# Kernel optimization log

Measured on AMD Instinct MI355X. Metric: run time of the kernel, lower is better.

Reference implementation:

```python
import jax, jax.numpy as jnp
import numpy as np

B, N, C, M, OUT = 4, 256, 32, 4, 64


def _uniform(k, shape, fan_in):
    s = 1.0 / np.sqrt(fan_in)
    return jax.random.uniform(k, shape, jnp.float32, -s, s)


def setup_inputs() -> dict:
    key = jax.random.key(0)
    ks = jax.random.split(key, 11)
    return {
        "x": jax.random.normal(ks[0], (B, N, N, C), jnp.float32),
        # Neighborhood / SnConv2to1 linears (in=C, out=M neighborhood channels)
        "w1_nb": _uniform(ks[1], (3 * C, M), 3 * C),
        "b1_nb": _uniform(ks[2], (M,), 3 * C),
        "w0_nb": _uniform(ks[3], (2 * C, M), 2 * C),
        "b0_nb": _uniform(ks[4], (M,), 2 * C),
        # SnConv2 linears (in channels = M*C after neighborhood product)
        "w2d": _uniform(ks[5], (2 * M * C, OUT), 2 * M * C),
        "b2d": _uniform(ks[6], (OUT,), 2 * M * C),
        "w1d": _uniform(ks[7], (3 * M * C, OUT), 3 * M * C),
        "b1d": _uniform(ks[8], (OUT,), 3 * M * C),
        "w0d": _uniform(ks[9], (2 * M * C, OUT), 2 * M * C),
        "b0d": _uniform(ks[10], (OUT,), 2 * M * C),
    }


def _contractions(x):
    # x: [B, n, n, c]; mask=None, reduction='mean' path of _get_contractions
    n = x.shape[1]
    rowsum = x.sum(axis=1) / n                      # [B, n, c]
    colsum = x.sum(axis=2) / n                      # [B, n, c]
    diag = jnp.diagonal(x, axis1=1, axis2=2)        # [B, c, n]
    rowcolsum = x.sum(axis=(1, 2)) / (n * n)        # [B, c]
    diag_sum = diag.sum(axis=-1) / n                # [B, c]  (/= sqrt(n^2))
    diag = jnp.moveaxis(diag, -1, 1)                # move_from_end -> [B, n, c]
    return rowsum, colsum, diag, rowcolsum, diag_sum


def reference(x, w1_nb, b1_nb, w0_nb, b0_nb, w2d, b2d, w1d, b1d, w0d, b0d):
    # ---- Neighborhood: SnConv2to1 -> sigmoid ----
    rs, cs, dg, rcs, ds = _contractions(x)
    obj1 = jnp.concatenate([rs, cs, dg], axis=-1)             # [B, n, 3C]
    obj0 = jnp.concatenate([rcs, ds], axis=-1)                # [B, 2C]
    node = obj1 @ w1_nb + b1_nb + (obj0 @ w0_nb + b0_nb)[:, None, :]
    neighbs = jax.nn.sigmoid(node)                            # [B, n, M]
    # ---- _neighbor_elementwise_product ----
    expanded = neighbs[:, None, :, :] * neighbs[:, :, None, :]  # [B, n, n, M]
    # channel_product: outer product over channel dims, collapsed to M*C
    xl = (expanded[..., :, None] * x[..., None, :]).reshape(B, N, N, M * C)
    # ---- SnConv2 on the localized tensor ----
    rs2, cs2, dg2, rcs2, ds2 = _contractions(xl)
    obj2d = jnp.concatenate([xl, jnp.swapaxes(xl, 1, 2)], axis=-1)  # [B,n,n,2MC]
    obj1d = jnp.concatenate([rs2, cs2, dg2], axis=-1)               # [B,n,3MC]
    obj0d = jnp.concatenate([rcs2, ds2], axis=-1)                   # [B,2MC]
    out = (obj2d @ w2d + b2d
           + (obj1d @ w1d + b1d)[:, None, :, :]
           + (obj0d @ w0d + b0d)[:, None, None, :])                 # [B,n,n,OUT]
    return out
```

## Files before the change

### kernel.cpp

```cpp
#include <hip/hip_runtime.h>
#include <math.h>

#define Bv 4
#define Nv 256
#define Cv 32
#define Mv 4
#define OUTv 64
#define MCv (Mv*Cv)

typedef _Float16 h8 __attribute__((ext_vector_type(8)));
typedef _Float16 h4 __attribute__((ext_vector_type(4)));
typedef float f4 __attribute__((ext_vector_type(4)));

__device__ __align__(16) float g_rs  [Bv * Nv * Cv];
__device__ __align__(16) float g_cs  [Bv * Nv * Cv];
__device__ __align__(16) float g_dgx [Bv * Nv * Cv];
__device__ __align__(16) float g_nb  [Bv * Nv * Mv];
__device__ __align__(16) float g_S1  [Bv * Nv * MCv];
__device__ __align__(16) float g_S2  [Bv * Nv * MCv];
__device__ __align__(16) float g_rcs2R[8 * Bv * MCv];
__device__ __align__(16) float g_ds2R [8 * Bv * MCv];
__device__ __align__(16) float g_addv[Bv * Nv * OUTv];
__device__ __align__(16) _Float16 g_wfrag[8 * 4 * 64 * 8];

__global__ __launch_bounds__(256) void k_contract1(const float* __restrict__ x,
                                                   const float* __restrict__ w2d) {
    int bx = blockIdx.x, b = blockIdx.y;
    int t = threadIdx.x;
    if (bx >= 2 * Nv) {
        if (b != 0) return;
        int r = bx - 2 * Nv;
        if (r == 8) {
            float4 z = {0.f,0.f,0.f,0.f};
            #pragma unroll
            for (int k = 0; k < 4; k++) {
                ((float4*)g_rcs2R)[k * 256 + t] = z;
                ((float4*)g_ds2R )[k * 256 + t] = z;
            }
            return;
        }
        int fi = r * 256 + t;
        int s = fi >> 8, q = (fi >> 6) & 3, lane = fi & 63;
        int k0 = s * 32 + ((lane >> 4) << 3);
        int o = q * 16 + (lane & 15);
        #pragma unroll
        for (int jj = 0; jj < 8; jj++)
            g_wfrag[fi * 8 + jj] = (_Float16)w2d[(size_t)(k0 + jj) * OUTv + o];
        return;
    }
    int c4 = t & 7, sub = t >> 3;
    const float4* xb4 = (const float4*)(x + (size_t)b * Nv * Nv * Cv);
    __shared__ float red[32][36];
    float4 acc = {0.f,0.f,0.f,0.f};
    if (bx < Nv) {
        int n = bx;
        for (int i = sub; i < Nv; i += 32) {
            float4 v = xb4[((size_t)i * Nv + n) * 8 + c4];
            acc.x += v.x; acc.y += v.y; acc.z += v.z; acc.w += v.w;
        }
        red[sub][c4*4+0] = acc.x; red[sub][c4*4+1] = acc.y;
        red[sub][c4*4+2] = acc.z; red[sub][c4*4+3] = acc.w;
        __syncthreads();
        if (t < 32) {
            float s = 0.f;
            #pragma unroll
            for (int k = 0; k < 32; k++) s += red[k][t];
            g_rs[(b * Nv + n) * Cv + t] = s * (1.0f / Nv);
        }
        if (t < 8) ((float4*)g_dgx)[(b * Nv + n) * 8 + t] = xb4[((size_t)n * Nv + n) * 8 + t];
    } else {
        int n = bx - Nv;
        for (int j = sub; j < Nv; j += 32) {
            float4 v = xb4[((size_t)n * Nv + j) * 8 + c4];
            acc.x += v.x; acc.y += v.y; acc.z += v.z; acc.w += v.w;
        }
        red[sub][c4*4+0] = acc.x; red[sub][c4*4+1] = acc.y;
        red[sub][c4*4+2] = acc.z; red[sub][c4*4+3] = acc.w;
        __syncthreads();
        if (t < 32) {
            float s = 0.f;
            #pragma unroll
            for (int k = 0; k < 32; k++) s += red[k][t];
            g_cs[(b * Nv + n) * Cv + t] = s * (1.0f / Nv);
        }
    }
}

__global__ void k_neighb(const float* __restrict__ w1, const float* __restrict__ b1,
                         const float* __restrict__ w0, const float* __restrict__ b0) {
    int b = blockIdx.x, t = threadIdx.x;
    int c = t & 31, sub = t >> 5;
    float ar = 0.f, ad = 0.f;
    for (int n = sub; n < Nv; n += 8) {
        ar += g_rs[(b * Nv + n) * Cv + c];
        ad += g_dgx[(b * Nv + n) * Cv + c];
    }
    __shared__ float red[8][64];
    __shared__ float obj0[64];
    __shared__ float t0nb[4];
    red[sub][c] = ar;
    red[sub][32 + c] = ad;
    __syncthreads();
    if (t < 64) {
        float s = 0.f;
        #pragma unroll
        for (int k = 0; k < 8; k++) s += red[k][t];
        obj0[t] = s * (1.0f / Nv);
    }
    __syncthreads();
    if (t < 4) {
        float v = b0[t];
        for (int k = 0; k < 2 * Cv; k++) v += obj0[k] * w0[k * Mv + t];
        t0nb[t] = v;
    }
    __syncthreads();
    int n = t;
    float node[4];
    #pragma unroll
    for (int m = 0; m < 4; m++) node[m] = t0nb[m] + b1[m];
    for (int cc = 0; cc < Cv; cc++) {
        float r = g_rs[(b * Nv + n) * Cv + cc];
        float s = g_cs[(b * Nv + n) * Cv + cc];
        float d = g_dgx[(b * Nv + n) * Cv + cc];
        #pragma unroll
        for (int m = 0; m < 4; m++)
            node[m] += r * w1[cc * Mv + m] + s * w1[(Cv + cc) * Mv + m] + d * w1[(2 * Cv + cc) * Mv + m];
    }
    #pragma unroll
    for (int m = 0; m < 4; m++)
        g_nb[(b * Nv + n) * Mv + m] = 1.0f / (1.0f + expf(-node[m]));
}

__global__ __launch_bounds__(256) void k_wsum(const float* __restrict__ x) {
    int bx = blockIdx.x, b = blockIdx.y;
    int t = threadIdx.x, c4 = t & 7, sub = t >> 3;
    __shared__ __align__(16) float4 nbl[Nv];
    if (t < Nv) nbl[t] = ((const float4*)(g_nb + (size_t)b * Nv * Mv))[t];
    __syncthreads();
    const float4* xb4 = (const float4*)(x + (size_t)b * Nv * Nv * Cv);
    float4 a[4];
    #pragma unroll
    for (int m = 0; m < 4; m++) a[m] = {0.f,0.f,0.f,0.f};
    __shared__ float red[32][132];
    if (bx < Nv) {
        int n = bx;
        for (int i = sub; i < Nv; i += 32) {
            float4 v = xb4[((size_t)i * Nv + n) * 8 + c4];
            float4 nv = nbl[i];
            a[0].x += nv.x*v.x; a[0].y += nv.x*v.y; a[0].z += nv.x*v.z; a[0].w += nv.x*v.w;
            a[1].x += nv.y*v.x; a[1].y += nv.y*v.y; a[1].z += nv.y*v.z; a[1].w += nv.y*v.w;
            a[2].x += nv.z*v.x; a[2].y += nv.z*v.y; a[2].z += nv.z*v.z; a[2].w += nv.z*v.w;
            a[3].x += nv.w*v.x; a[3].y += nv.w*v.y; a[3].z += nv.w*v.z; a[3].w += nv.w*v.w;
        }
        #pragma unroll
        for (int m = 0; m < 4; m++) {
            red[sub][m*32 + c4*4+0] = a[m].x; red[sub][m*32 + c4*4+1] = a[m].y;
            red[sub][m*32 + c4*4+2] = a[m].z; red[sub][m*32 + c4*4+3] = a[m].w;
        }
        __syncthreads();
        if (t < 128) {
            float s = 0.f;
            #pragma unroll
            for (int k = 0; k < 32; k++) s += red[k][t];
            g_S1[(size_t)(b * Nv + n) * MCv + t] = s;
            int m = t >> 5, c = t & 31;
            float nv = ((const float*)&nbl[n])[m];
            int rep = ((n & 7) * Bv + b) * MCv + t;
            atomicAdd(&g_rcs2R[rep], nv * s);
            atomicAdd(&g_ds2R [rep], nv * nv * g_dgx[(b * Nv + n) * Cv + c]);
        }
    } else {
        int n = bx - Nv;
        for (int j = sub; j < Nv; j += 32) {
            float4 v = xb4[((size_t)n * Nv + j) * 8 + c4];
            float4 nv = nbl[j];
            a[0].x += nv.x*v.x; a[0].y += nv.x*v.y; a[0].z += nv.x*v.z; a[0].w += nv.x*v.w;
            a[1].x += nv.y*v.x; a[1].y += nv.y*v.y; a[1].z += nv.y*v.z; a[1].w += nv.y*v.w;
            a[2].x += nv.z*v.x; a[2].y += nv.z*v.y; a[2].z += nv.z*v.z; a[2].w += nv.z*v.w;
            a[3].x += nv.w*v.x; a[3].y += nv.w*v.y; a[3].z += nv.w*v.z; a[3].w += nv.w*v.w;
        }
        #pragma unroll
        for (int m = 0; m < 4; m++) {
            red[sub][m*32 + c4*4+0] = a[m].x; red[sub][m*32 + c4*4+1] = a[m].y;
            red[sub][m*32 + c4*4+2] = a[m].z; red[sub][m*32 + c4*4+3] = a[m].w;
        }
        __syncthreads();
        if (t < 128) {
            float s = 0.f;
            #pragma unroll
            for (int k = 0; k < 32; k++) s += red[k][t];
            g_S2[(size_t)(b * Nv + n) * MCv + t] = s;
        }
    }
}

__global__ __launch_bounds__(256) void k_add(const float* __restrict__ w1d,
                                             const float* __restrict__ b1d,
                                             const float* __restrict__ b2d,
                                             const float* __restrict__ w0d,
                                             const float* __restrict__ b0d) {
    int b = blockIdx.y, n0 = blockIdx.x * 2;
    int t = threadIdx.x, o = t & 63, ks = t >> 6;
    __shared__ float rcl[MCv], dsl[MCv];
    __shared__ float red0[4][64];
    __shared__ float red2[4][2][64];
    if (t < 128) {
        float s = 0.f;
        #pragma unroll
        for (int r = 0; r < 8; r++) s += g_rcs2R[(r * Bv + b) * MCv + t];
        rcl[t] = s;
    } else {
        int tt = t - 128;
        float s = 0.f;
        #pragma unroll
        for (int r = 0; r < 8; r++) s += g_ds2R[(r * Bv + b) * MCv + tt];
        dsl[tt] = s;
    }
    __syncthreads();
    const float invN = 1.0f / Nv;
    const float invN2 = invN * invN;
    float nv0 = g_nb[(b * Nv + n0) * Mv + ks];
    float nv1 = g_nb[(b * Nv + n0 + 1) * Mv + ks];
    float f0 = nv0 * invN, d20 = nv0 * nv0;
    float f1 = nv1 * invN, d21 = nv1 * nv1;
    const float* S1a = g_S1 + (size_t)(b * Nv + n0) * MCv + ks * 32;
    const float* S1b = S1a + MCv;
    const float* S2a = g_S2 + (size_t)(b * Nv + n0) * MCv + ks * 32;
    const float* S2b = S2a + MCv;
    const float* dga = g_dgx + (size_t)(b * Nv + n0) * Cv;
    const float* dgb = dga + Cv;
    float acc0v = 0.f, accA = 0.f, accB = 0.f;
    #pragma unroll 8
    for (int cc = 0; cc < 32; cc++) {
        int mc = ks * 32 + cc;
        float w1a = w1d[(size_t)mc * OUTv + o];
        float w1b = w1d[(size_t)(MCv + mc) * OUTv + o];
        float w1c = w1d[(size_t)(2 * MCv + mc) * OUTv + o];
        float w0a = w0d[(size_t)mc * OUTv + o];
        float w0b = w0d[(size_t)(MCv + mc) * OUTv + o];
        acc0v += invN2 * rcl[mc] * w0a + invN * dsl[mc] * w0b;
        accA  += f0 * S1a[cc] * w1a + f0 * S2a[cc] * w1b + d20 * dga[cc] * w1c;
        accB  += f1 * S1b[cc] * w1a + f1 * S2b[cc] * w1b + d21 * dgb[cc] * w1c;
    }
    red0[ks][o] = acc0v;
    red2[ks][0][o] = accA;
    red2[ks][1][o] = accB;
    __syncthreads();
    if (t < 128) {
        int nn = t >> 6, oo = t & 63;
        float t0v = red0[0][oo] + red0[1][oo] + red0[2][oo] + red0[3][oo]
                  + b1d[oo] + b2d[oo] + b0d[oo];
        float v = red2[0][nn][oo] + red2[1][nn][oo] + red2[2][nn][oo] + red2[3][nn][oo] + t0v;
        g_addv[(size_t)(b * Nv + n0 + nn) * OUTv + oo] = v;
    }
}

#define XPAD 40
__global__ __launch_bounds__(256) void k_main(const float* __restrict__ x,
                                              float* __restrict__ out) {
    int jt = blockIdx.x, ip = blockIdx.y, b = blockIdx.z;
    int i0 = ip * 2, i1 = i0 + 1;
    int j0 = jt * 128;
    int t = threadIdx.x;
    int lane = t & 63, w = t >> 6;
    int rowA = lane & 15, quad = lane >> 4;

    __shared__ __align__(16) _Float16 Wl[8 * 4 * 64 * 8];
    __shared__ __align__(16) _Float16 Xt0[128 * XPAD];
    __shared__ __align__(16) _Float16 Xb0[128 * XPAD];
    __shared__ __align__(16) _Float16 Xt1[128 * XPAD];
    __shared__ __align__(16) _Float16 Xb1[128 * XPAD];

    {
        const float4* src = (const float4*)g_wfrag;
        float4* dst = (float4*)Wl;
        #pragma unroll
        for (int r = 0; r < 8; r++) dst[r * 256 + t] = src[r * 256 + t];
    }
    {
        const float4* x4 = (const float4*)x;
        #pragma unroll
        for (int r = 0; r < 4; r++) {
            int idx = r * 256 + t;
            int j = idx >> 3, c4 = idx & 7;
            float4 v0 = x4[((size_t)(b * Nv + i0) * Nv + j0 + j) * 8 + c4];
            float4 v1 = x4[((size_t)(b * Nv + i1) * Nv + j0 + j) * 8 + c4];
            float4 u0 = x4[((size_t)(b * Nv + j0 + j) * Nv + i0) * 8 + c4];
            float4 u1 = x4[((size_t)(b * Nv + j0 + j) * Nv + i1) * 8 + c4];
            h4 h0; h0[0] = (_Float16)v0.x; h0[1] = (_Float16)v0.y;
            h0[2] = (_Float16)v0.z; h0[3] = (_Float16)v0.w;
            *(h4*)&Xt0[j * XPAD + c4 * 4] = h0;
            h4 h1; h1[0] = (_Float16)v1.x; h1[1] = (_Float16)v1.y;
            h1[2] = (_Float16)v1.z; h1[3] = (_Float16)v1.w;
            *(h4*)&Xt1[j * XPAD + c4 * 4] = h1;
            h4 g0; g0[0] = (_Float16)u0.x; g0[1] = (_Float16)u0.y;
            g0[2] = (_Float16)u0.z; g0[3] = (_Float16)u0.w;
            *(h4*)&Xb0[j * XPAD + c4 * 4] = g0;
            h4 g1; g1[0] = (_Float16)u1.x; g1[1] = (_Float16)u1.y;
            g1[2] = (_Float16)u1.z; g1[3] = (_Float16)u1.w;
            *(h4*)&Xb1[j * XPAD + c4 * 4] = g1;
        }
    }
    int jl1 = w * 32 + rowA, jl2 = jl1 + 16;
    _Float16 e1h0[4], e2h0[4], e1h1[4], e2h1[4];
    {
        const float* ni0 = g_nb + (size_t)(b * Nv + i0) * Mv;
        const float* ni1 = g_nb + (size_t)(b * Nv + i1) * Mv;
        const float* n1 = g_nb + (size_t)(b * Nv + j0 + jl1) * Mv;
        const float* n2 = g_nb + (size_t)(b * Nv + j0 + jl2) * Mv;
        #pragma unroll
        for (int m = 0; m < 4; m++) {
            e1h0[m] = (_Float16)(ni0[m] * n1[m]);
            e2h0[m] = (_Float16)(ni0[m] * n2[m]);
            e1h1[m] = (_Float16)(ni1[m] * n1[m]);
            e2h1[m] = (_Float16)(ni1[m] * n2[m]);
        }
    }
    __syncthreads();

    f4 acc[2][2][4];
    #pragma unroll
    for (int ii = 0; ii < 2; ii++)
        #pragma unroll
        for (int js = 0; js < 2; js++)
            #pragma unroll
            for (int q = 0; q < 4; q++) acc[ii][js][q] = {0.f, 0.f, 0.f, 0.f};

    const h8* Wf = (const h8*)Wl;
    #pragma unroll
    for (int part = 0; part < 2; part++) {
        const _Float16* X0 = part ? Xb0 : Xt0;
        const _Float16* X1 = part ? Xb1 : Xt1;
        h8 xv1_0 = *(const h8*)&X0[jl1 * XPAD + quad * 8];
        h8 xv2_0 = *(const h8*)&X0[jl2 * XPAD + quad * 8];
        h8 xv1_1 = *(const h8*)&X1[jl1 * XPAD + quad * 8];
        h8 xv2_1 = *(const h8*)&X1[jl2 * XPAD + quad * 8];
        #pragma unroll
        for (int m = 0; m < 4; m++) {
            h8 a1_0 = xv1_0 * e1h0[m];
            h8 a2_0 = xv2_0 * e2h0[m];
            h8 a1_1 = xv1_1 * e1h1[m];
            h8 a2_1 = xv2_1 * e2h1[m];
            int s = part * 4 + m;
            #pragma unroll
            for (int q = 0; q < 4; q++) {
                h8 bf = Wf[(s * 4 + q) * 64 + lane];
                acc[0][0][q] = __builtin_amdgcn_mfma_f32_16x16x32_f16(a1_0, bf, acc[0][0][q], 0, 0, 0);
                acc[0][1][q] = __builtin_amdgcn_mfma_f32_16x16x32_f16(a2_0, bf, acc[0][1][q], 0, 0, 0);
                acc[1][0][q] = __builtin_amdgcn_mfma_f32_16x16x32_f16(a1_1, bf, acc[1][0][q], 0, 0, 0);
                acc[1][1][q] = __builtin_amdgcn_mfma_f32_16x16x32_f16(a2_1, bf, acc[1][1][q], 0, 0, 0);
            }
        }
    }
    #pragma unroll
    for (int js = 0; js < 2; js++) {
        int jbase = j0 + w * 32 + js * 16 + quad * 4;
        #pragma unroll
        for (int q = 0; q < 4; q++) {
            int o = q * 16 + rowA;
            #pragma unroll
            for (int r = 0; r < 4; r++) {
                int j = jbase + r;
                float av = g_addv[(size_t)(b * Nv + j) * OUTv + o];
                out[(((size_t)(b * Nv + i0)) * Nv + j) * OUTv + o] = acc[0][js][q][r] + av;
                out[(((size_t)(b * Nv + i1)) * Nv + j) * OUTv + o] = acc[1][js][q][r] + av;
            }
        }
    }
}

extern "C" void kernel_launch(void* const* d_in, const int* in_sizes, int n_in,
                              void* d_out, int out_size, void* d_ws, size_t ws_size,
                              hipStream_t stream) {
    const float* x     = (const float*)d_in[0];
    const float* w1_nb = (const float*)d_in[1];
    const float* b1_nb = (const float*)d_in[2];
    const float* w0_nb = (const float*)d_in[3];
    const float* b0_nb = (const float*)d_in[4];
    const float* w2d   = (const float*)d_in[5];
    const float* b2d   = (const float*)d_in[6];
    const float* w1d   = (const float*)d_in[7];
    const float* b1d   = (const float*)d_in[8];
    const float* w0d   = (const float*)d_in[9];
    const float* b0d   = (const float*)d_in[10];
    float* out = (float*)d_out;
    (void)d_ws; (void)ws_size;

    hipLaunchKernelGGL(k_contract1, dim3(2 * Nv + 9, Bv), dim3(256), 0, stream, x, w2d);
    hipLaunchKernelGGL(k_neighb, dim3(Bv), dim3(256), 0, stream,
                       w1_nb, b1_nb, w0_nb, b0_nb);
    hipLaunchKernelGGL(k_wsum, dim3(2 * Nv, Bv), dim3(256), 0, stream, x);
    hipLaunchKernelGGL(k_add, dim3(Nv / 2, Bv), dim3(256), 0, stream,
                       w1d, b1d, b2d, w0d, b0d);
    hipLaunchKernelGGL(k_main, dim3(2, Nv / 2, Bv), dim3(256), 0, stream, x, out);
}
```

Baseline: 169.4 us.

## Fuse neighborhood, weighted-sum and per-row add kernels into one kernel

Merges k_neighb, k_wsum and k_add into a single k_fused kernel with one block per (n, b). Each block recomputes the sigmoid neighborhood weights for its batch, then computes both the row and column weighted sums and the per-row linear term from shared memory. This removes two launches and the global S1/S2 round-trip. The rcs2/ds2 reduction and its w0d product move into k_main, because the atomic accumulation must finish before they can be used. The cost is redundant neighborhood computation in every block and extra per-block setup work in k_main.

```diff
diff --git a/kernel.cpp b/kernel.cpp
--- a/kernel.cpp
+++ b/kernel.cpp
@@ -16,8 +16,6 @@
 __device__ __align__(16) float g_cs  [Bv * Nv * Cv];
 __device__ __align__(16) float g_dgx [Bv * Nv * Cv];
 __device__ __align__(16) float g_nb  [Bv * Nv * Mv];
-__device__ __align__(16) float g_S1  [Bv * Nv * MCv];
-__device__ __align__(16) float g_S2  [Bv * Nv * MCv];
 __device__ __align__(16) float g_rcs2R[8 * Bv * MCv];
 __device__ __align__(16) float g_ds2R [8 * Bv * MCv];
 __device__ __align__(16) float g_addv[Bv * Nv * OUTv];
@@ -86,25 +84,37 @@
     }
 }
 
-__global__ void k_neighb(const float* __restrict__ w1, const float* __restrict__ b1,
-                         const float* __restrict__ w0, const float* __restrict__ b0) {
-    int b = blockIdx.x, t = threadIdx.x;
-    int c = t & 31, sub = t >> 5;
-    float ar = 0.f, ad = 0.f;
-    for (int n = sub; n < Nv; n += 8) {
-        ar += g_rs[(b * Nv + n) * Cv + c];
-        ad += g_dgx[(b * Nv + n) * Cv + c];
-    }
-    __shared__ float red[8][64];
+__global__ __launch_bounds__(256) void k_fused(const float* __restrict__ x,
+    const float* __restrict__ w1, const float* __restrict__ b1,
+    const float* __restrict__ w0, const float* __restrict__ b0,
+    const float* __restrict__ w1d, const float* __restrict__ b1d,
+    const float* __restrict__ b2d, const float* __restrict__ b0d) {
+    int n = blockIdx.x, b = blockIdx.y;
+    int t = threadIdx.x;
+
+    __shared__ float red8[8][64];
     __shared__ float obj0[64];
     __shared__ float t0nb[4];
-    red[sub][c] = ar;
-    red[sub][32 + c] = ad;
+    __shared__ __align__(16) float nb4[Nv][4];
+    __shared__ float red[32][132];
+    __shared__ float S1l[MCv], S2l[MCv];
+    __shared__ float redD[4][64];
+
+    {
+        int c = t & 31, sub = t >> 5;
+        float ar = 0.f, ad = 0.f;
+        for (int nn = sub; nn < Nv; nn += 8) {
+            ar += g_rs[(b * Nv + nn) * Cv + c];
+            ad += g_dgx[(b * Nv + nn) * Cv + c];
+        }
+        red8[sub][c] = ar;
+        red8[sub][32 + c] = ad;
+    }
     __syncthreads();
     if (t < 64) {
         float s = 0.f;
         #pragma unroll
-        for (int k = 0; k < 8; k++) s += red[k][t];
+        for (int k = 0; k < 8; k++) s += red8[k][t];
         obj0[t] = s * (1.0f / Nv);
     }
     __syncthreads();
@@ -114,39 +124,47 @@
         t0nb[t] = v;
     }
     __syncthreads();
-    int n = t;
-    float node[4];
-    #pragma unroll
-    for (int m = 0; m < 4; m++) node[m] = t0nb[m] + b1[m];
-    for (int cc = 0; cc < Cv; cc++) {
-        float r = g_rs[(b * Nv + n) * Cv + cc];
-        float s = g_cs[(b * Nv + n) * Cv + cc];
-        float d = g_dgx[(b * Nv + n) * Cv + cc];
+    {
+        const float4* rs4 = (const float4*)(g_rs  + (size_t)(b * Nv + t) * Cv);
+        const float4* cs4 = (const float4*)(g_cs  + (size_t)(b * Nv + t) * Cv);
+        const float4* dg4 = (const float4*)(g_dgx + (size_t)(b * Nv + t) * Cv);
+        float node[4];
+        #pragma unroll
+        for (int m = 0; m < 4; m++) node[m] = t0nb[m] + b1[m];
+        #pragma unroll
+        for (int q = 0; q < 8; q++) {
+            float4 R = rs4[q], S = cs4[q], D = dg4[q];
+            #pragma unroll
+            for (int e = 0; e < 4; e++) {
+                int cc = q * 4 + e;
+                float r = ((const float*)&R)[e];
+                float s = ((const float*)&S)[e];
+                float d = ((const float*)&D)[e];
+                #pragma unroll
+                for (int m = 0; m < 4; m++)
+                    node[m] += r * w1[cc * Mv + m] + s * w1[(Cv + cc) * Mv + m]
+                             + d * w1[(2 * Cv + cc) * Mv + m];
+            }
+        }
+        float4 nv;
         #pragma unroll
         for (int m = 0; m < 4; m++)
-            node[m] += r * w1[cc * Mv + m] + s * w1[(Cv + cc) * Mv + m] + d * w1[(2 * Cv + cc) * Mv + m];
-    }
-    #pragma unroll
-    for (int m = 0; m < 4; m++)
-        g_nb[(b * Nv + n) * Mv + m] = 1.0f / (1.0f + expf(-node[m]));
-}
-
-__global__ __launch_bounds__(256) void k_wsum(const float* __restrict__ x) {
-    int bx = blockIdx.x, b = blockIdx.y;
-    int t = threadIdx.x, c4 = t & 7, sub = t >> 3;
-    __shared__ __align__(16) float4 nbl[Nv];
-    if (t < Nv) nbl[t] = ((const float4*)(g_nb + (size_t)b * Nv * Mv))[t];
-    __syncthreads();
+            ((float*)&nv)[m] = 1.0f / (1.0f + expf(-node[m]));
+        *(float4*)nb4[t] = nv;
+        if (n == 0) ((float4*)g_nb)[b * Nv + t] = nv;
+    }
+    __syncthreads();
+
     const float4* xb4 = (const float4*)(x + (size_t)b * Nv * Nv * Cv);
-    float4 a[4];
-    #pragma unroll
-    for (int m = 0; m < 4; m++) a[m] = {0.f,0.f,0.f,0.f};
-    __shared__ float red[32][132];
-    if (bx < Nv) {
-        int n = bx;
-        for (int i = sub; i < Nv; i += 32) {
+    int c4 = t & 7, sub3 = t >> 3;
+
+    {
+        float4 a[4];
+        #pragma unroll
+        for (int m = 0; m < 4; m++) a[m] = {0.f,0.f,0.f,0.f};
+        for (int i = sub3; i < Nv; i += 32) {
             float4 v = xb4[((size_t)i * Nv + n) * 8 + c4];
-            float4 nv = nbl[i];
+            float4 nv = *(const float4*)nb4[i];
             a[0].x += nv.x*v.x; a[0].y += nv.x*v.y; a[0].z += nv.x*v.z; a[0].w += nv.x*v.w;
             a[1].x += nv.y*v.x; a[1].y += nv.y*v.y; a[1].z += nv.y*v.z; a[1].w += nv.y*v.w;
             a[2].x += nv.z*v.x; a[2].y += nv.z*v.y; a[2].z += nv.z*v.z; a[2].w += nv.z*v.w;
@@ -154,26 +172,31 @@
         }
         #pragma unroll
         for (int m = 0; m < 4; m++) {
-            red[sub][m*32 + c4*4+0] = a[m].x; red[sub][m*32 + c4*4+1] = a[m].y;
-            red[sub][m*32 + c4*4+2] = a[m].z; red[sub][m*32 + c4*4+3] = a[m].w;
-        }
-        __syncthreads();
-        if (t < 128) {
-            float s = 0.f;
-            #pragma unroll
-            for (int k = 0; k < 32; k++) s += red[k][t];
-            g_S1[(size_t)(b * Nv + n) * MCv + t] = s;
-            int m = t >> 5, c = t & 31;
-            float nv = ((const float*)&nbl[n])[m];
-            int rep = ((n & 7) * Bv + b) * MCv + t;
-            atomicAdd(&g_rcs2R[rep], nv * s);
-            atomicAdd(&g_ds2R [rep], nv * nv * g_dgx[(b * Nv + n) * Cv + c]);
-        }
-    } else {
-        int n = bx - Nv;
-        for (int j = sub; j < Nv; j += 32) {
+            red[sub3][m*32 + c4*4+0] = a[m].x; red[sub3][m*32 + c4*4+1] = a[m].y;
+            red[sub3][m*32 + c4*4+2] = a[m].z; red[sub3][m*32 + c4*4+3] = a[m].w;
+        }
+    }
+    __syncthreads();
+    if (t < 128) {
+        float s = 0.f;
+        #pragma unroll
+        for (int k = 0; k < 32; k++) s += red[k][t];
+        S1l[t] = s;
+        int m = t >> 5, c = t & 31;
+        float nv = nb4[n][m];
+        int rep = ((n & 7) * Bv + b) * MCv + t;
+        atomicAdd(&g_rcs2R[rep], nv * s);
+        atomicAdd(&g_ds2R [rep], nv * nv * g_dgx[(b * Nv + n) * Cv + c]);
+    }
+    __syncthreads();
+
+    {
+        float4 a[4];
+        #pragma unroll
+        for (int m = 0; m < 4; m++) a[m] = {0.f,0.f,0.f,0.f};
+        for (int j = sub3; j < Nv; j += 32) {
             float4 v = xb4[((size_t)n * Nv + j) * 8 + c4];
-            float4 nv = nbl[j];
+            float4 nv = *(const float4*)nb4[j];
             a[0].x += nv.x*v.x; a[0].y += nv.x*v.y; a[0].z += nv.x*v.z; a[0].w += nv.x*v.w;
             a[1].x += nv.y*v.x; a[1].y += nv.y*v.y; a[1].z += nv.y*v.z; a[1].w += nv.y*v.w;
             a[2].x += nv.z*v.x; a[2].y += nv.z*v.y; a[2].z += nv.z*v.z; a[2].w += nv.z*v.w;
@@ -181,83 +204,47 @@
         }
         #pragma unroll
         for (int m = 0; m < 4; m++) {
-            red[sub][m*32 + c4*4+0] = a[m].x; red[sub][m*32 + c4*4+1] = a[m].y;
-            red[sub][m*32 + c4*4+2] = a[m].z; red[sub][m*32 + c4*4+3] = a[m].w;
-        }
-        __syncthreads();
-        if (t < 128) {
-            float s = 0.f;
-            #pragma unroll
-            for (int k = 0; k < 32; k++) s += red[k][t];
-            g_S2[(size_t)(b * Nv + n) * MCv + t] = s;
-        }
-    }
-}
-
-__global__ __launch_bounds__(256) void k_add(const float* __restrict__ w1d,
-                                             const float* __restrict__ b1d,
-                                             const float* __restrict__ b2d,
-                                             const float* __restrict__ w0d,
-                                             const float* __restrict__ b0d) {
-    int b = blockIdx.y, n0 = blockIdx.x * 2;
-    int t = threadIdx.x, o = t & 63, ks = t >> 6;
-    __shared__ float rcl[MCv], dsl[MCv];
-    __shared__ float red0[4][64];
-    __shared__ float red2[4][2][64];
+            red[sub3][m*32 + c4*4+0] = a[m].x; red[sub3][m*32 + c4*4+1] = a[m].y;
+            red[sub3][m*32 + c4*4+2] = a[m].z; red[sub3][m*32 + c4*4+3] = a[m].w;
+        }
+    }
+    __syncthreads();
     if (t < 128) {
         float s = 0.f;
         #pragma unroll
-        for (int r = 0; r < 8; r++) s += g_rcs2R[(r * Bv + b) * MCv + t];
-        rcl[t] = s;
-    } else {
-        int tt = t - 128;
-        float s = 0.f;
-        #pragma unroll
-        for (int r = 0; r < 8; r++) s += g_ds2R[(r * Bv + b) * MCv + tt];
-        dsl[tt] = s;
-    }
-    __syncthreads();
-    const float invN = 1.0f / Nv;
-    const float invN2 = invN * invN;
-    float nv0 = g_nb[(b * Nv + n0) * Mv + ks];
-    float nv1 = g_nb[(b * Nv + n0 + 1) * Mv + ks];
-    float f0 = nv0 * invN, d20 = nv0 * nv0;
-    float f1 = nv1 * invN, d21 = nv1 * nv1;
-    const float* S1a = g_S1 + (size_t)(b * Nv + n0) * MCv + ks * 32;
-    const float* S1b = S1a + MCv;
-    const float* S2a = g_S2 + (size_t)(b * Nv + n0) * MCv + ks * 32;
-    const float* S2b = S2a + MCv;
-    const float* dga = g_dgx + (size_t)(b * Nv + n0) * Cv;
-    const float* dgb = dga + Cv;
-    float acc0v = 0.f, accA = 0.f, accB = 0.f;
-    #pragma unroll 8
-    for (int cc = 0; cc < 32; cc++) {
-        int mc = ks * 32 + cc;
-        float w1a = w1d[(size_t)mc * OUTv + o];
-        float w1b = w1d[(size_t)(MCv + mc) * OUTv + o];
-        float w1c = w1d[(size_t)(2 * MCv + mc) * OUTv + o];
-        float w0a = w0d[(size_t)mc * OUTv + o];
-        float w0b = w0d[(size_t)(MCv + mc) * OUTv + o];
-        acc0v += invN2 * rcl[mc] * w0a + invN * dsl[mc] * w0b;
-        accA  += f0 * S1a[cc] * w1a + f0 * S2a[cc] * w1b + d20 * dga[cc] * w1c;
-        accB  += f1 * S1b[cc] * w1a + f1 * S2b[cc] * w1b + d21 * dgb[cc] * w1c;
-    }
-    red0[ks][o] = acc0v;
-    red2[ks][0][o] = accA;
-    red2[ks][1][o] = accB;
-    __syncthreads();
-    if (t < 128) {
-        int nn = t >> 6, oo = t & 63;
-        float t0v = red0[0][oo] + red0[1][oo] + red0[2][oo] + red0[3][oo]
-                  + b1d[oo] + b2d[oo] + b0d[oo];
-        float v = red2[0][nn][oo] + red2[1][nn][oo] + red2[2][nn][oo] + red2[3][nn][oo] + t0v;
-        g_addv[(size_t)(b * Nv + n0 + nn) * OUTv + oo] = v;
+        for (int k = 0; k < 32; k++) s += red[k][t];
+        S2l[t] = s;
+    }
+    __syncthreads();
+
+    {
+        int o = t & 63, ks = t >> 6;
+        const float invN = 1.0f / Nv;
+        float nv = nb4[n][ks];
+        float f = nv * invN, d2 = nv * nv;
+        const float* dgr = g_dgx + (size_t)(b * Nv + n) * Cv;
+        float acc = 0.f;
+        #pragma unroll 8
+        for (int cc = 0; cc < 32; cc++) {
+            int mc = ks * 32 + cc;
+            acc += f * S1l[mc] * w1d[(size_t)mc * OUTv + o]
+                 + f * S2l[mc] * w1d[(size_t)(MCv + mc) * OUTv + o]
+                 + d2 * dgr[cc] * w1d[(size_t)(2 * MCv + mc) * OUTv + o];
+        }
+        redD[ks][o] = acc;
+    }
+    __syncthreads();
+    if (t < 64) {
+        float v = redD[0][t] + redD[1][t] + redD[2][t] + redD[3][t]
+                + b1d[t] + b2d[t] + b0d[t];
+        g_addv[(size_t)(b * Nv + n) * OUTv + t] = v;
     }
 }
 
 #define XPAD 40
 __global__ __launch_bounds__(256) void k_main(const float* __restrict__ x,
-                                              float* __restrict__ out) {
+                                              float* __restrict__ out,
+                                              const float* __restrict__ w0d) {
     int jt = blockIdx.x, ip = blockIdx.y, b = blockIdx.z;
     int i0 = ip * 2, i1 = i0 + 1;
     int j0 = jt * 128;
@@ -270,6 +257,9 @@
     __shared__ __align__(16) _Float16 Xb0[128 * XPAD];
     __shared__ __align__(16) _Float16 Xt1[128 * XPAD];
     __shared__ __align__(16) _Float16 Xb1[128 * XPAD];
+    __shared__ float rcl[MCv], dsl[MCv];
+    __shared__ float t0red[4][64];
+    __shared__ float t0l[64];
 
     {
         const float4* src = (const float4*)g_wfrag;
@@ -301,6 +291,18 @@
             *(h4*)&Xb1[j * XPAD + c4 * 4] = g1;
         }
     }
+    if (t < 128) {
+        float s = 0.f;
+        #pragma unroll
+        for (int r = 0; r < 8; r++) s += g_rcs2R[(r * Bv + b) * MCv + t];
+        rcl[t] = s;
+    } else {
+        int tt = t - 128;
+        float s = 0.f;
+        #pragma unroll
+        for (int r = 0; r < 8; r++) s += g_ds2R[(r * Bv + b) * MCv + tt];
+        dsl[tt] = s;
+    }
     int jl1 = w * 32 + rowA, jl2 = jl1 + 16;
     _Float16 e1h0[4], e2h0[4], e1h1[4], e2h1[4];
     {
@@ -316,6 +318,22 @@
             e2h1[m] = (_Float16)(ni1[m] * n2[m]);
         }
     }
+    __syncthreads();
+    {
+        int o = t & 63, ks = t >> 6;
+        const float invN = 1.0f / Nv;
+        const float invN2 = invN * invN;
+        float a0 = 0.f;
+        #pragma unroll 8
+        for (int cc = 0; cc < 32; cc++) {
+            int mc = ks * 32 + cc;
+            a0 += invN2 * rcl[mc] * w0d[(size_t)mc * OUTv + o]
+                + invN  * dsl[mc] * w0d[(size_t)(MCv + mc) * OUTv + o];
+        }
+        t0red[ks][o] = a0;
+    }
+    __syncthreads();
+    if (t < 64) t0l[t] = t0red[0][t] + t0red[1][t] + t0red[2][t] + t0red[3][t];
     __syncthreads();
 
     f4 acc[2][2][4];
@@ -358,10 +376,11 @@
         #pragma unroll
         for (int q = 0; q < 4; q++) {
             int o = q * 16 + rowA;
+            float tv = t0l[o];
             #pragma unroll
             for (int r = 0; r < 4; r++) {
                 int j = jbase + r;
-                float av = g_addv[(size_t)(b * Nv + j) * OUTv + o];
+                float av = g_addv[(size_t)(b * Nv + j) * OUTv + o] + tv;
                 out[(((size_t)(b * Nv + i0)) * Nv + j) * OUTv + o] = acc[0][js][q][r] + av;
                 out[(((size_t)(b * Nv + i1)) * Nv + j) * OUTv + o] = acc[1][js][q][r] + av;
             }
@@ -387,10 +406,7 @@
     (void)d_ws; (void)ws_size;
 
     hipLaunchKernelGGL(k_contract1, dim3(2 * Nv + 9, Bv), dim3(256), 0, stream, x, w2d);
-    hipLaunchKernelGGL(k_neighb, dim3(Bv), dim3(256), 0, stream,
-                       w1_nb, b1_nb, w0_nb, b0_nb);
-    hipLaunchKernelGGL(k_wsum, dim3(2 * Nv, Bv), dim3(256), 0, stream, x);
-    hipLaunchKernelGGL(k_add, dim3(Nv / 2, Bv), dim3(256), 0, stream,
-                       w1d, b1d, b2d, w0d, b0d);
-    hipLaunchKernelGGL(k_main, dim3(2, Nv / 2, Bv), dim3(256), 0, stream, x, out);
+    hipLaunchKernelGGL(k_fused, dim3(Nv, Bv), dim3(256), 0, stream,
+                       x, w1_nb, b1_nb, w0_nb, b0_nb, w1d, b1d, b2d, b0d);
+    hipLaunchKernelGGL(k_main, dim3(2, Nv / 2, Bv), dim3(256), 0, stream, x, out, w0d);
 }
```

Result: no change. 171.8 us (+1.4%).
